# Kernel optimization log

Hardware: AMD Instinct MI355X
Metric: run time of the kernel (lower is better)

## Reference

```python
import jax, jax.numpy as jnp
import numpy as np


def cosine_noise_schedule(t):
    # legacy mode: 1 - cos(t/1.008 * pi/2)^2
    return 1.0 - jnp.cos(t / 1.008 * jnp.pi / 2.0) ** 2


def setup_inputs() -> dict:
    key = jax.random.key(0)
    k1, k2, k3 = jax.random.split(key, 3)
    x = jax.random.normal(k1, (256, 3, 32, 32), dtype=jnp.float32)
    images = jax.random.normal(k2, (50000, 3, 32, 32), dtype=jnp.float32)
    t = jax.random.uniform(k3, (1,), dtype=jnp.float32)
    return {"t": t, "x": x, "images": images}


def reference(t, x, images):
    # Exact ideal score: softmax over dataset of Gaussian kernel weights.
    # The original streams dataset batches with an online-softmax running max;
    # with uniform batch sizes that is mathematically a global softmax over N:
    #   score = -(x - at * E_p[y]) / bt^2,  p_j = softmax(-||x - at*y_j||^2 / (2 bt^2))
    sched = cosine_noise_schedule(t)          # [1]
    bt = jnp.sqrt(sched)                      # [1]
    at = jnp.sqrt(1.0 - sched)                # [1]
    b, c, h, w = x.shape
    n = images.shape[0]
    xf = x.reshape(b, -1)                     # [b, chw]
    yf = images.reshape(n, -1)                # [n, chw]
    # ||x - at*y||^2 = ||x||^2 + at^2 ||y||^2 - 2 at x.y  (GEMM-dominant)
    x2 = jnp.sum(xf * xf, axis=1)             # [b]
    y2 = jnp.sum(yf * yf, axis=1)             # [n]
    cross = xf @ yf.T                         # [b, n]
    d2 = x2[:, None] + (at ** 2) * y2[None, :] - 2.0 * at * cross  # [b, n]
    logits = -d2 / (2.0 * bt ** 2)            # [b, n]
    p = jax.nn.softmax(logits, axis=1)        # [b, n], stable (max-subtracted)
    ybar = (p @ yf).reshape(b, c, h, w)       # softmax-weighted dataset mean
    return -(x - at * ybar) / (bt ** 2)
```

## Files before the change

kernel.cpp:

```cpp
#include <hip/hip_runtime.h>

typedef float    f32x4  __attribute__((ext_vector_type(4)));
typedef float    f32x16 __attribute__((ext_vector_type(16)));
typedef _Float16 f16x4  __attribute__((ext_vector_type(4)));
typedef _Float16 f16x8  __attribute__((ext_vector_type(8)));

#define N_IMG 50000
#define BROWS 256
#define CHW   3072
#define BK    32
#define PITCH 40
#define BN    128
#define BM    128
#define KCHUNK 3136
#define NSPLIT 16

__global__ void k_scalars(const float* __restrict__ t, float* __restrict__ sc) {
    if (threadIdx.x == 0) {
        double tv  = (double)t[0];
        double ang = tv * (1.5707963267948966 / 1.008);
        double c   = cos(ang);
        double at  = c;
        double bt2 = 1.0 - c * c;
        sc[0] = (float)at;
        sc[1] = (float)bt2;
        sc[2] = (float)(at / bt2);
        sc[3] = (float)(at * at * 0.5 / bt2);
        sc[4] = (float)(1.0 / bt2);
    }
}

__global__ void k_xprep(const float* __restrict__ x, _Float16* __restrict__ xh) {
    int idx = blockIdx.x * 256 + threadIdx.x;
    f32x4 v = ((const f32x4*)x)[idx];
    f16x4 h;
    h[0] = (_Float16)v[0]; h[1] = (_Float16)v[1];
    h[2] = (_Float16)v[2]; h[3] = (_Float16)v[3];
    ((f16x4*)xh)[idx] = h;
}

__global__ __launch_bounds__(256, 4) void k_gemm1(
        const _Float16* __restrict__ xh, const float* __restrict__ img,
        const float* __restrict__ sc, float* __restrict__ logits) {
    __shared__ _Float16 Alds[BM * PITCH];
    __shared__ _Float16 Blds[BN * PITCH];
    __shared__ float y2lds[BN];

    const int tid = threadIdx.x;
    const int m0  = blockIdx.x * BM;
    const int n0  = blockIdx.y * BN;

    const int arow = tid >> 1;
    const int akk  = (tid & 1) * 16;
    const int brow = tid >> 1;
    const int bkk  = (tid & 1) * 16;
    const bool bvalid = (n0 + brow) < N_IMG;
    const _Float16* asrc = xh + (size_t)(m0 + arow) * CHW + akk;
    const float*    bsrc = img + (size_t)(n0 + brow) * CHW + bkk;

    f16x8 areg[2];
    f32x4 breg[4];
    float y2p = 0.f;
    const f32x4 fz = {0.f, 0.f, 0.f, 0.f};

    auto loadT = [&](int kt) {
        const f16x8* ap = (const f16x8*)(asrc + kt);
        areg[0] = ap[0]; areg[1] = ap[1];
        if (bvalid) {
            const f32x4* bp = (const f32x4*)(bsrc + kt);
            breg[0] = bp[0]; breg[1] = bp[1]; breg[2] = bp[2]; breg[3] = bp[3];
        } else {
            breg[0] = fz; breg[1] = fz; breg[2] = fz; breg[3] = fz;
        }
        #pragma unroll
        for (int i = 0; i < 4; i++)
            y2p += breg[i][0]*breg[i][0] + breg[i][1]*breg[i][1]
                 + breg[i][2]*breg[i][2] + breg[i][3]*breg[i][3];
    };
    auto storeT = [&]() {
        f16x8* adst = (f16x8*)&Alds[arow * PITCH + akk];
        adst[0] = areg[0]; adst[1] = areg[1];
        f16x8 b0, b1;
        #pragma unroll
        for (int j = 0; j < 4; j++) {
            b0[j]   = (_Float16)breg[0][j];
            b0[4+j] = (_Float16)breg[1][j];
            b1[j]   = (_Float16)breg[2][j];
            b1[4+j] = (_Float16)breg[3][j];
        }
        f16x8* bdst = (f16x8*)&Blds[brow * PITCH + bkk];
        bdst[0] = b0; bdst[1] = b1;
    };

    const int wid  = tid >> 6;
    const int lane = tid & 63;
    const int wm = wid >> 1, wn = wid & 1;
    const int rm = wm * 64, cn = wn * 64;
    const int lr = lane & 31, hi = lane >> 5;

    f32x16 acc[2][2];
    #pragma unroll
    for (int mi = 0; mi < 2; mi++)
        #pragma unroll
        for (int ni = 0; ni < 2; ni++)
            #pragma unroll
            for (int r = 0; r < 16; r++) acc[mi][ni][r] = 0.f;

    loadT(0);
    for (int it = 0; it < CHW / BK; ++it) {
        __syncthreads();
        storeT();
        __syncthreads();
        if (it + 1 < CHW / BK) loadT((it + 1) * BK);
        #pragma unroll
        for (int ks = 0; ks < 2; ++ks) {
            f16x8 a0 = *(const f16x8*)&Alds[(rm +      lr) * PITCH + ks*16 + hi*8];
            f16x8 a1 = *(const f16x8*)&Alds[(rm + 32 + lr) * PITCH + ks*16 + hi*8];
            f16x8 b0 = *(const f16x8*)&Blds[(cn +      lr) * PITCH + ks*16 + hi*8];
            f16x8 b1 = *(const f16x8*)&Blds[(cn + 32 + lr) * PITCH + ks*16 + hi*8];
            acc[0][0] = __builtin_amdgcn_mfma_f32_32x32x16_f16(a0, b0, acc[0][0], 0, 0, 0);
            acc[0][1] = __builtin_amdgcn_mfma_f32_32x32x16_f16(a0, b1, acc[0][1], 0, 0, 0);
            acc[1][0] = __builtin_amdgcn_mfma_f32_32x32x16_f16(a1, b0, acc[1][0], 0, 0, 0);
            acc[1][1] = __builtin_amdgcn_mfma_f32_32x32x16_f16(a1, b1, acc[1][1], 0, 0, 0);
        }
    }

    float s = y2p;
    s += __shfl_xor(s, 1);
    if ((tid & 1) == 0) y2lds[brow] = s;
    __syncthreads();

    const float c_cross = sc[2], c_y2 = sc[3];
    #pragma unroll
    for (int mi = 0; mi < 2; mi++)
        #pragma unroll
        for (int ni = 0; ni < 2; ni++) {
            int col = n0 + cn + ni * 32 + lr;
            if (col >= N_IMG) continue;
            float y2v = y2lds[cn + ni * 32 + lr];
            f32x16 v = acc[mi][ni];
            #pragma unroll
            for (int r = 0; r < 16; r++) {
                int row = m0 + rm + mi * 32 + (r & 3) + 8 * (r >> 2) + 4 * hi;
                logits[(size_t)row * N_IMG + col] = c_cross * v[r] - c_y2 * y2v;
            }
        }
}

__global__ void k_softmax(const float* __restrict__ logits, _Float16* __restrict__ eh,
                          float* __restrict__ rowsum) {
    int row = blockIdx.x, tid = threadIdx.x;
    const f32x4* lr = (const f32x4*)(logits + (size_t)row * N_IMG);
    f16x4* er = (f16x4*)(eh + (size_t)row * N_IMG);
    __shared__ float wred[4];

    float m = -3.0e38f;
    for (int i = tid; i < N_IMG / 4; i += 256) {
        f32x4 v = lr[i];
        m = fmaxf(m, fmaxf(fmaxf(v[0], v[1]), fmaxf(v[2], v[3])));
    }
    for (int o = 32; o > 0; o >>= 1) m = fmaxf(m, __shfl_down(m, o));
    if ((tid & 63) == 0) wred[tid >> 6] = m;
    __syncthreads();
    m = fmaxf(fmaxf(wred[0], wred[1]), fmaxf(wred[2], wred[3]));
    __syncthreads();

    float s = 0.f;
    for (int i = tid; i < N_IMG / 4; i += 256) {
        f32x4 v = lr[i];
        float e0 = __expf(v[0] - m), e1 = __expf(v[1] - m);
        float e2 = __expf(v[2] - m), e3 = __expf(v[3] - m);
        s += (e0 + e1) + (e2 + e3);
        f16x4 h;
        h[0] = (_Float16)e0; h[1] = (_Float16)e1;
        h[2] = (_Float16)e2; h[3] = (_Float16)e3;
        er[i] = h;
    }
    for (int o = 32; o > 0; o >>= 1) s += __shfl_down(s, o);
    if ((tid & 63) == 0) wred[tid >> 6] = s;
    __syncthreads();
    if (tid == 0) rowsum[row] = (wred[0] + wred[1]) + (wred[2] + wred[3]);
}

__global__ __launch_bounds__(256, 4) void k_gemm2(
        const _Float16* __restrict__ eh, const float* __restrict__ img,
        float* __restrict__ partial) {
    __shared__ _Float16 Alds[BM * PITCH];
    __shared__ _Float16 Blds[BN * PITCH];

    const int tid = threadIdx.x;
    const int m0  = blockIdx.x * BM;
    const int d0  = blockIdx.y * BN;
    const int ck  = blockIdx.z;
    const int kbase = ck * KCHUNK;
    const int kend  = (kbase + KCHUNK < N_IMG) ? (kbase + KCHUNK) : N_IMG;
    const int iters = (kend - kbase + BK - 1) / BK;

    const int arow = tid >> 1;
    const int akk  = (tid & 1) * 16;
    const _Float16* asrc = eh + (size_t)(m0 + arow) * N_IMG + akk;
    const int bd = (tid & 31) * 4;
    const int bq = (tid >> 5) * 4;

    f16x8 areg[2];
    f32x4 breg[4];
    const f16x8 hz = {(_Float16)0.f,(_Float16)0.f,(_Float16)0.f,(_Float16)0.f,
                      (_Float16)0.f,(_Float16)0.f,(_Float16)0.f,(_Float16)0.f};
    const f32x4 fz = {0.f, 0.f, 0.f, 0.f};

    auto loadT = [&](int kt) {
        #pragma unroll
        for (int j = 0; j < 2; j++) {
            int gk = kt + akk + j * 8;
            areg[j] = (gk < N_IMG) ? *(const f16x8*)(asrc + kt + j * 8) : hz;
        }
        #pragma unroll
        for (int i = 0; i < 4; i++) {
            int gk = kt + bq + i;
            breg[i] = (gk < N_IMG) ? *(const f32x4*)(img + (size_t)gk * CHW + d0 + bd) : fz;
        }
    };
    auto storeT = [&]() {
        f16x8* adst = (f16x8*)&Alds[arow * PITCH + akk];
        adst[0] = areg[0]; adst[1] = areg[1];
        #pragma unroll
        for (int j = 0; j < 4; j++) {
            f16x4 h;
            h[0] = (_Float16)breg[0][j]; h[1] = (_Float16)breg[1][j];
            h[2] = (_Float16)breg[2][j]; h[3] = (_Float16)breg[3][j];
            *(f16x4*)&Blds[(bd + j) * PITCH + bq] = h;
        }
    };

    const int wid  = tid >> 6;
    const int lane = tid & 63;
    const int wm = wid >> 1, wn = wid & 1;
    const int rm = wm * 64, cn = wn * 64;
    const int lr = lane & 31, hi = lane >> 5;

    f32x16 acc[2][2];
    #pragma unroll
    for (int mi = 0; mi < 2; mi++)
        #pragma unroll
        for (int ni = 0; ni < 2; ni++)
            #pragma unroll
            for (int r = 0; r < 16; r++) acc[mi][ni][r] = 0.f;

    loadT(kbase);
    for (int it = 0; it < iters; ++it) {
        __syncthreads();
        storeT();
        __syncthreads();
        if (it + 1 < iters) loadT(kbase + (it + 1) * BK);
        #pragma unroll
        for (int ks = 0; ks < 2; ++ks) {
            f16x8 a0 = *(const f16x8*)&Alds[(rm +      lr) * PITCH + ks*16 + hi*8];
            f16x8 a1 = *(const f16x8*)&Alds[(rm + 32 + lr) * PITCH + ks*16 + hi*8];
            f16x8 b0 = *(const f16x8*)&Blds[(cn +      lr) * PITCH + ks*16 + hi*8];
            f16x8 b1 = *(const f16x8*)&Blds[(cn + 32 + lr) * PITCH + ks*16 + hi*8];
            acc[0][0] = __builtin_amdgcn_mfma_f32_32x32x16_f16(a0, b0, acc[0][0], 0, 0, 0);
            acc[0][1] = __builtin_amdgcn_mfma_f32_32x32x16_f16(a0, b1, acc[0][1], 0, 0, 0);
            acc[1][0] = __builtin_amdgcn_mfma_f32_32x32x16_f16(a1, b0, acc[1][0], 0, 0, 0);
            acc[1][1] = __builtin_amdgcn_mfma_f32_32x32x16_f16(a1, b1, acc[1][1], 0, 0, 0);
        }
    }

    float* pp = partial + (size_t)ck * BROWS * CHW;
    #pragma unroll
    for (int mi = 0; mi < 2; mi++)
        #pragma unroll
        for (int ni = 0; ni < 2; ni++) {
            int dcol = d0 + cn + ni * 32 + lr;
            f32x16 v = acc[mi][ni];
            #pragma unroll
            for (int r = 0; r < 16; r++) {
                int row = m0 + rm + mi * 32 + (r & 3) + 8 * (r >> 2) + 4 * hi;
                pp[(size_t)row * CHW + dcol] = v[r];
            }
        }
}

__global__ void k_final(const float* __restrict__ partial, const float* __restrict__ x,
                        const float* __restrict__ rowsum, const float* __restrict__ sc,
                        float* __restrict__ out) {
    int idx = blockIdx.x * 256 + threadIdx.x;
    int row = idx / (CHW / 4);
    float at = sc[0], invbt2 = sc[4];
    float scale = at * invbt2 / rowsum[row];
    const f32x4* p4 = (const f32x4*)partial;
    f32x4 s = p4[idx];
    #pragma unroll
    for (int c = 1; c < NSPLIT; c++) s = s + p4[(size_t)c * (BROWS * CHW / 4) + idx];
    f32x4 xv = ((const f32x4*)x)[idx];
    f32x4 o;
    #pragma unroll
    for (int j = 0; j < 4; j++) o[j] = s[j] * scale - xv[j] * invbt2;
    ((f32x4*)out)[idx] = o;
}

extern "C" void kernel_launch(void* const* d_in, const int* in_sizes, int n_in,
                              void* d_out, int out_size, void* d_ws, size_t ws_size,
                              hipStream_t stream) {
    const float* t   = (const float*)d_in[0];
    const float* x   = (const float*)d_in[1];
    const float* img = (const float*)d_in[2];
    float* out = (float*)d_out;
    char* ws = (char*)d_ws;

    float*    sc     = (float*)(ws + 0);
    float*    rowsum = (float*)(ws + 2560);
    _Float16* xh     = (_Float16*)(ws + 4096);
    _Float16* eh     = (_Float16*)(ws + 4096 + 1572864);
    float*    logits = (float*)(ws + 4096 + 1572864 + 25600000);
    float*    partial = logits;

    k_scalars<<<1, 64, 0, stream>>>(t, sc);
    k_xprep<<<(BROWS * CHW / 4) / 256, 256, 0, stream>>>(x, xh);
    k_gemm1<<<dim3(2, (N_IMG + BN - 1) / BN), 256, 0, stream>>>(xh, img, sc, logits);
    k_softmax<<<256, 256, 0, stream>>>(logits, eh, rowsum);
    k_gemm2<<<dim3(2, CHW / BN, NSPLIT), 256, 0, stream>>>(eh, img, partial);
    k_final<<<(BROWS * CHW / 4) / 256, 256, 0, stream>>>(partial, x, rowsum, sc, out);
}
```

Baseline: 566.6 us.

## Pre-convert images to fp16 once and stream GEMM tiles via direct global-to-LDS loads

```diff
diff --git a/kernel.cpp b/kernel.cpp
--- a/kernel.cpp
+++ b/kernel.cpp
@@ -8,12 +8,18 @@
 #define N_IMG 50000
 #define BROWS 256
 #define CHW   3072
-#define BK    32
-#define PITCH 40
+#define BK    64
+#define BM    128
 #define BN    128
-#define BM    128
+#define EHS   50176
 #define KCHUNK 3136
 #define NSPLIT 16
+
+__device__ __forceinline__ void glds16(const void* g, void* l) {
+    __builtin_amdgcn_global_load_lds(
+        (const __attribute__((address_space(1))) void*)g,
+        (__attribute__((address_space(3))) void*)l, 16, 0, 0);
+}
 
 __global__ void k_scalars(const float* __restrict__ t, float* __restrict__ sc) {
     if (threadIdx.x == 0) {
@@ -39,64 +45,63 @@
     ((f16x4*)xh)[idx] = h;
 }
 
-__global__ __launch_bounds__(256, 4) void k_gemm1(
-        const _Float16* __restrict__ xh, const float* __restrict__ img,
-        const float* __restrict__ sc, float* __restrict__ logits) {
-    __shared__ _Float16 Alds[BM * PITCH];
-    __shared__ _Float16 Blds[BN * PITCH];
-    __shared__ float y2lds[BN];
+__global__ void k_prep(const float* __restrict__ img, _Float16* __restrict__ imgh,
+                       float* __restrict__ y2) {
+    int row = blockIdx.x, tid = threadIdx.x;
+    const f32x4* src = (const f32x4*)(img + (size_t)row * CHW);
+    f16x4* dst = (f16x4*)(imgh + (size_t)row * CHW);
+    float s = 0.f;
+    #pragma unroll
+    for (int i = 0; i < 3; i++) {
+        f32x4 v = src[tid + i * 256];
+        s += v[0]*v[0] + v[1]*v[1] + v[2]*v[2] + v[3]*v[3];
+        f16x4 h;
+        h[0] = (_Float16)v[0]; h[1] = (_Float16)v[1];
+        h[2] = (_Float16)v[2]; h[3] = (_Float16)v[3];
+        dst[tid + i * 256] = h;
+    }
+    for (int o = 32; o > 0; o >>= 1) s += __shfl_down(s, o);
+    __shared__ float wsum[4];
+    if ((tid & 63) == 0) wsum[tid >> 6] = s;
+    __syncthreads();
+    if (tid == 0) y2[row] = (wsum[0] + wsum[1]) + (wsum[2] + wsum[3]);
+}
+
+__global__ __launch_bounds__(256, 3) void k_gemm1(
+        const _Float16* __restrict__ xh, const _Float16* __restrict__ imgh,
+        const float* __restrict__ y2g, const float* __restrict__ sc,
+        float* __restrict__ logits) {
+    __shared__ _Float16 Alds[BM * BK];
+    __shared__ _Float16 Blds[BN * BK];
 
     const int tid = threadIdx.x;
-    const int m0  = blockIdx.x * BM;
-    const int n0  = blockIdx.y * BN;
-
-    const int arow = tid >> 1;
-    const int akk  = (tid & 1) * 16;
-    const int brow = tid >> 1;
-    const int bkk  = (tid & 1) * 16;
-    const bool bvalid = (n0 + brow) < N_IMG;
-    const _Float16* asrc = xh + (size_t)(m0 + arow) * CHW + akk;
-    const float*    bsrc = img + (size_t)(n0 + brow) * CHW + bkk;
-
-    f16x8 areg[2];
-    f32x4 breg[4];
-    float y2p = 0.f;
-    const f32x4 fz = {0.f, 0.f, 0.f, 0.f};
-
-    auto loadT = [&](int kt) {
-        const f16x8* ap = (const f16x8*)(asrc + kt);
-        areg[0] = ap[0]; areg[1] = ap[1];
-        if (bvalid) {
-            const f32x4* bp = (const f32x4*)(bsrc + kt);
-            breg[0] = bp[0]; breg[1] = bp[1]; breg[2] = bp[2]; breg[3] = bp[3];
-        } else {
-            breg[0] = fz; breg[1] = fz; breg[2] = fz; breg[3] = fz;
-        }
-        #pragma unroll
-        for (int i = 0; i < 4; i++)
-            y2p += breg[i][0]*breg[i][0] + breg[i][1]*breg[i][1]
-                 + breg[i][2]*breg[i][2] + breg[i][3]*breg[i][3];
-    };
-    auto storeT = [&]() {
-        f16x8* adst = (f16x8*)&Alds[arow * PITCH + akk];
-        adst[0] = areg[0]; adst[1] = areg[1];
-        f16x8 b0, b1;
-        #pragma unroll
-        for (int j = 0; j < 4; j++) {
-            b0[j]   = (_Float16)breg[0][j];
-            b0[4+j] = (_Float16)breg[1][j];
-            b1[j]   = (_Float16)breg[2][j];
-            b1[4+j] = (_Float16)breg[3][j];
-        }
-        f16x8* bdst = (f16x8*)&Blds[brow * PITCH + bkk];
-        bdst[0] = b0; bdst[1] = b1;
-    };
-
-    const int wid  = tid >> 6;
-    const int lane = tid & 63;
+    const int wid = tid >> 6, lane = tid & 63;
+    const int m0 = blockIdx.x * BM;
+    const int n0 = blockIdx.y * BN;
+
+    const _Float16* gA[4]; const _Float16* gB[4];
+    _Float16* lA[4]; _Float16* lB[4];
+    #pragma unroll
+    for (int j = 0; j < 4; j++) {
+        int seg = wid * 4 + j;
+        int row = seg * 8 + (lane >> 3);
+        int off = (((lane & 7) ^ (row & 7)) << 3);
+        gA[j] = xh + (size_t)(m0 + row) * CHW + off;
+        int rb = n0 + row; if (rb > N_IMG - 1) rb = N_IMG - 1;
+        gB[j] = imgh + (size_t)rb * CHW + off;
+        lA[j] = Alds + seg * 512;
+        lB[j] = Blds + seg * 512;
+    }
+
     const int wm = wid >> 1, wn = wid & 1;
     const int rm = wm * 64, cn = wn * 64;
     const int lr = lane & 31, hi = lane >> 5;
+    const int xm = (lr & 7) << 4;
+    const char* Ab = (const char*)Alds;
+    const char* Bb = (const char*)Blds;
+    const int ar0 = (rm + lr) * 128,      ar1 = (rm + 32 + lr) * 128;
+    const int br0 = (cn + lr) * 128,      br1 = (cn + 32 + lr) * 128;
+    const int kof = hi * 16;
 
     f32x16 acc[2][2];
     #pragma unroll
@@ -106,18 +111,20 @@
             #pragma unroll
             for (int r = 0; r < 16; r++) acc[mi][ni][r] = 0.f;
 
-    loadT(0);
     for (int it = 0; it < CHW / BK; ++it) {
+        if (it) __syncthreads();
+        #pragma unroll
+        for (int j = 0; j < 4; j++) glds16(gA[j] + it * BK, lA[j]);
+        #pragma unroll
+        for (int j = 0; j < 4; j++) glds16(gB[j] + it * BK, lB[j]);
         __syncthreads();
-        storeT();
-        __syncthreads();
-        if (it + 1 < CHW / BK) loadT((it + 1) * BK);
-        #pragma unroll
-        for (int ks = 0; ks < 2; ++ks) {
-            f16x8 a0 = *(const f16x8*)&Alds[(rm +      lr) * PITCH + ks*16 + hi*8];
-            f16x8 a1 = *(const f16x8*)&Alds[(rm + 32 + lr) * PITCH + ks*16 + hi*8];
-            f16x8 b0 = *(const f16x8*)&Blds[(cn +      lr) * PITCH + ks*16 + hi*8];
-            f16x8 b1 = *(const f16x8*)&Blds[(cn + 32 + lr) * PITCH + ks*16 + hi*8];
+        #pragma unroll
+        for (int ks = 0; ks < 4; ++ks) {
+            int off = (ks * 32 + kof) ^ xm;
+            f16x8 a0 = *(const f16x8*)(Ab + ar0 + off);
+            f16x8 a1 = *(const f16x8*)(Ab + ar1 + off);
+            f16x8 b0 = *(const f16x8*)(Bb + br0 + off);
+            f16x8 b1 = *(const f16x8*)(Bb + br1 + off);
             acc[0][0] = __builtin_amdgcn_mfma_f32_32x32x16_f16(a0, b0, acc[0][0], 0, 0, 0);
             acc[0][1] = __builtin_amdgcn_mfma_f32_32x32x16_f16(a0, b1, acc[0][1], 0, 0, 0);
             acc[1][0] = __builtin_amdgcn_mfma_f32_32x32x16_f16(a1, b0, acc[1][0], 0, 0, 0);
@@ -125,11 +132,6 @@
         }
     }
 
-    float s = y2p;
-    s += __shfl_xor(s, 1);
-    if ((tid & 1) == 0) y2lds[brow] = s;
-    __syncthreads();
-
     const float c_cross = sc[2], c_y2 = sc[3];
     #pragma unroll
     for (int mi = 0; mi < 2; mi++)
@@ -137,7 +139,7 @@
         for (int ni = 0; ni < 2; ni++) {
             int col = n0 + cn + ni * 32 + lr;
             if (col >= N_IMG) continue;
-            float y2v = y2lds[cn + ni * 32 + lr];
+            float y2v = y2g[col];
             f32x16 v = acc[mi][ni];
             #pragma unroll
             for (int r = 0; r < 16; r++) {
@@ -151,8 +153,11 @@
                           float* __restrict__ rowsum) {
     int row = blockIdx.x, tid = threadIdx.x;
     const f32x4* lr = (const f32x4*)(logits + (size_t)row * N_IMG);
-    f16x4* er = (f16x4*)(eh + (size_t)row * N_IMG);
+    _Float16* erow = eh + (size_t)row * EHS;
+    f16x4* er = (f16x4*)erow;
     __shared__ float wred[4];
+
+    if (tid < EHS - N_IMG) erow[N_IMG + tid] = (_Float16)0.f;
 
     float m = -3.0e38f;
     for (int i = tid; i < N_IMG / 4; i += 256) {
@@ -182,61 +187,57 @@
     if (tid == 0) rowsum[row] = (wred[0] + wred[1]) + (wred[2] + wred[3]);
 }
 
-__global__ __launch_bounds__(256, 4) void k_gemm2(
-        const _Float16* __restrict__ eh, const float* __restrict__ img,
+__global__ __launch_bounds__(256, 3) void k_gemm2(
+        const _Float16* __restrict__ eh, const _Float16* __restrict__ imgh,
         float* __restrict__ partial) {
-    __shared__ _Float16 Alds[BM * PITCH];
-    __shared__ _Float16 Blds[BN * PITCH];
+    __shared__ _Float16 Alds[BM * BK];
+    __shared__ _Float16 Blds[BN * 72];
 
     const int tid = threadIdx.x;
-    const int m0  = blockIdx.x * BM;
-    const int d0  = blockIdx.y * BN;
-    const int ck  = blockIdx.z;
+    const int wid = tid >> 6, lane = tid & 63;
+    const int m0 = blockIdx.x * BM;
+    const int d0 = blockIdx.y * BN;
+    const int ck = blockIdx.z;
     const int kbase = ck * KCHUNK;
     const int kend  = (kbase + KCHUNK < N_IMG) ? (kbase + KCHUNK) : N_IMG;
     const int iters = (kend - kbase + BK - 1) / BK;
 
-    const int arow = tid >> 1;
-    const int akk  = (tid & 1) * 16;
-    const _Float16* asrc = eh + (size_t)(m0 + arow) * N_IMG + akk;
+    const _Float16* gA[4]; _Float16* lA[4];
+    #pragma unroll
+    for (int j = 0; j < 4; j++) {
+        int seg = wid * 4 + j;
+        int row = seg * 8 + (lane >> 3);
+        int off = (((lane & 7) ^ (row & 7)) << 3);
+        gA[j] = eh + (size_t)(m0 + row) * EHS + kbase + off;
+        lA[j] = Alds + seg * 512;
+    }
     const int bd = (tid & 31) * 4;
-    const int bq = (tid >> 5) * 4;
-
-    f16x8 areg[2];
-    f32x4 breg[4];
-    const f16x8 hz = {(_Float16)0.f,(_Float16)0.f,(_Float16)0.f,(_Float16)0.f,
-                      (_Float16)0.f,(_Float16)0.f,(_Float16)0.f,(_Float16)0.f};
-    const f32x4 fz = {0.f, 0.f, 0.f, 0.f};
-
-    auto loadT = [&](int kt) {
-        #pragma unroll
-        for (int j = 0; j < 2; j++) {
-            int gk = kt + akk + j * 8;
-            areg[j] = (gk < N_IMG) ? *(const f16x8*)(asrc + kt + j * 8) : hz;
-        }
-        #pragma unroll
-        for (int i = 0; i < 4; i++) {
-            int gk = kt + bq + i;
-            breg[i] = (gk < N_IMG) ? *(const f32x4*)(img + (size_t)gk * CHW + d0 + bd) : fz;
+    const int bq = (tid >> 5) * 8;
+    f16x4 breg[8];
+    auto loadB = [&](int kt) {
+        #pragma unroll
+        for (int i = 0; i < 8; i++) {
+            int k = kt + bq + i; if (k > N_IMG - 1) k = N_IMG - 1;
+            breg[i] = *(const f16x4*)(imgh + (size_t)k * CHW + d0 + bd);
         }
     };
-    auto storeT = [&]() {
-        f16x8* adst = (f16x8*)&Alds[arow * PITCH + akk];
-        adst[0] = areg[0]; adst[1] = areg[1];
+    auto storeB = [&]() {
         #pragma unroll
         for (int j = 0; j < 4; j++) {
-            f16x4 h;
-            h[0] = (_Float16)breg[0][j]; h[1] = (_Float16)breg[1][j];
-            h[2] = (_Float16)breg[2][j]; h[3] = (_Float16)breg[3][j];
-            *(f16x4*)&Blds[(bd + j) * PITCH + bq] = h;
+            f16x8 w;
+            #pragma unroll
+            for (int i = 0; i < 8; i++) w[i] = breg[i][j];
+            *(f16x8*)&Blds[(bd + j) * 72 + bq] = w;
         }
     };
 
-    const int wid  = tid >> 6;
-    const int lane = tid & 63;
     const int wm = wid >> 1, wn = wid & 1;
     const int rm = wm * 64, cn = wn * 64;
     const int lr = lane & 31, hi = lane >> 5;
+    const int xm = (lr & 7) << 4;
+    const char* Ab = (const char*)Alds;
+    const int ar0 = (rm + lr) * 128, ar1 = (rm + 32 + lr) * 128;
+    const int kof = hi * 16;
 
     f32x16 acc[2][2];
     #pragma unroll
@@ -246,18 +247,22 @@
             #pragma unroll
             for (int r = 0; r < 16; r++) acc[mi][ni][r] = 0.f;
 
-    loadT(kbase);
+    loadB(kbase);
     for (int it = 0; it < iters; ++it) {
+        if (it) __syncthreads();
+        #pragma unroll
+        for (int j = 0; j < 4; j++) glds16(gA[j] + it * BK, lA[j]);
+        storeB();
         __syncthreads();
-        storeT();
-        __syncthreads();
-        if (it + 1 < iters) loadT(kbase + (it + 1) * BK);
-        #pragma unroll
-        for (int ks = 0; ks < 2; ++ks) {
-            f16x8 a0 = *(const f16x8*)&Alds[(rm +      lr) * PITCH + ks*16 + hi*8];
-            f16x8 a1 = *(const f16x8*)&Alds[(rm + 32 + lr) * PITCH + ks*16 + hi*8];
-            f16x8 b0 = *(const f16x8*)&Blds[(cn +      lr) * PITCH + ks*16 + hi*8];
-            f16x8 b1 = *(const f16x8*)&Blds[(cn + 32 + lr) * PITCH + ks*16 + hi*8];
+        if (it + 1 < iters) loadB(kbase + (it + 1) * BK);
+        #pragma unroll
+        for (int ks = 0; ks < 4; ++ks) {
+            int offa = (ks * 32 + kof) ^ xm;
+            int offb = ks * 16 + hi * 8;
+            f16x8 a0 = *(const f16x8*)(Ab + ar0 + offa);
+            f16x8 a1 = *(const f16x8*)(Ab + ar1 + offa);
+            f16x8 b0 = *(const f16x8*)&Blds[(cn +      lr) * 72 + offb];
+            f16x8 b1 = *(const f16x8*)&Blds[(cn + 32 + lr) * 72 + offb];
             acc[0][0] = __builtin_amdgcn_mfma_f32_32x32x16_f16(a0, b0, acc[0][0], 0, 0, 0);
             acc[0][1] = __builtin_amdgcn_mfma_f32_32x32x16_f16(a0, b1, acc[0][1], 0, 0, 0);
             acc[1][0] = __builtin_amdgcn_mfma_f32_32x32x16_f16(a1, b0, acc[1][0], 0, 0, 0);
@@ -308,16 +313,19 @@
     char* ws = (char*)d_ws;
 
     float*    sc     = (float*)(ws + 0);
-    float*    rowsum = (float*)(ws + 2560);
-    _Float16* xh     = (_Float16*)(ws + 4096);
-    _Float16* eh     = (_Float16*)(ws + 4096 + 1572864);
-    float*    logits = (float*)(ws + 4096 + 1572864 + 25600000);
+    float*    rowsum = (float*)(ws + 256);
+    float*    y2     = (float*)(ws + 4096);
+    _Float16* xh     = (_Float16*)(ws + 212992);
+    _Float16* imgh   = (_Float16*)(ws + 2097152);
+    _Float16* eh     = (_Float16*)(ws + 311427072);
+    float*    logits = (float*)(ws + 337117184);
     float*    partial = logits;
 
     k_scalars<<<1, 64, 0, stream>>>(t, sc);
     k_xprep<<<(BROWS * CHW / 4) / 256, 256, 0, stream>>>(x, xh);
-    k_gemm1<<<dim3(2, (N_IMG + BN - 1) / BN), 256, 0, stream>>>(xh, img, sc, logits);
+    k_prep<<<N_IMG, 256, 0, stream>>>(img, imgh, y2);
+    k_gemm1<<<dim3(2, (N_IMG + BN - 1) / BN), 256, 0, stream>>>(xh, imgh, y2, sc, logits);
     k_softmax<<<256, 256, 0, stream>>>(logits, eh, rowsum);
-    k_gemm2<<<dim3(2, CHW / BN, NSPLIT), 256, 0, stream>>>(eh, img, partial);
+    k_gemm2<<<dim3(2, CHW / BN, NSPLIT), 256, 0, stream>>>(eh, imgh, partial);
     k_final<<<(BROWS * CHW / 4) / 256, 256, 0, stream>>>(partial, x, rowsum, sc, out);
 }
```

New measurement: 490.3 us. 1.16x faster.
